# Optimization experiments

Measured on AMD Instinct MI355X. Metric: run time of the kernel, lower is better.

Reference implementation:

```python
import jax, jax.numpy as jnp
import numpy as np

B, C, T = 2, 64, 800
D, H, DH, FFD, L, NC = 128, 8, 64, 512, 2, 4
PL, NW = 25, 32            # patch_length, num_windows
WD = 0.1                   # window_duration
AHD = H * DH               # 512
SCALE = DH ** -0.5


def setup_inputs() -> dict:
    key = jax.random.key(0)
    ks = iter(jax.random.split(key, 40))
    def nrm(shape, s=0.02):
        return jax.random.normal(next(ks), shape, jnp.float32) * s
    return {
        "x_eeg": jax.random.normal(next(ks), (B, C, T), jnp.float32),
        "epoch_start_times": jax.random.uniform(next(ks), (B,), jnp.float32) * 10.0,
        "channel_voxel_indices": jax.random.randint(next(ks), (B, C), 0, 2048),
        "conv_w": nrm((D, PL), 0.1), "conv_b": nrm((D,), 0.01),
        "cls_token": nrm((1, 1, D), 1.0), "cls_pos": nrm((1, 1, D), 1.0),
        "bias_time_e": nrm((H, DH)), "bias_time_r": nrm((H, DH)),
        "bias_channel_r": nrm((H, DH)), "bias_channel_e": nrm((H, DH)),
        "ln1_g": jnp.ones((L, D)), "ln1_b": jnp.zeros((L, D)),
        "wqkv": nrm((L, D, 3 * AHD)), "wkt": nrm((L, D, AHD)), "wkc": nrm((L, D, AHD)),
        "wo": nrm((L, AHD, D)), "bo": jnp.zeros((L, D)),
        "ln2_g": jnp.ones((L, D)), "ln2_b": jnp.zeros((L, D)),
        "w1": nrm((L, D, FFD)), "b1": jnp.zeros((L, FFD)),
        "w2": nrm((L, FFD, D)), "b2": jnp.zeros((L, D)),
        "head_ln_g": jnp.ones((D,)), "head_ln_b": jnp.zeros((D,)),
        "head_w": nrm((D, NC)), "head_b": jnp.zeros((NC,)),
    }


def _ln(x, g, b, eps=1e-5):
    m = x.mean(-1, keepdims=True)
    v = ((x - m) ** 2).mean(-1, keepdims=True)
    return (x - m) / jnp.sqrt(v + eps) * g + b


def _posemb(p):
    # sinusoidal: outer product with inverse frequencies, concat(sin, cos)
    inv = 1.0 / (10000.0 ** (jnp.arange(0, D, 2, dtype=jnp.float32) / D))
    op = p[..., None] * inv
    return jnp.concatenate([jnp.sin(op), jnp.cos(op)], -1)


def reference(x_eeg, epoch_start_times, channel_voxel_indices, conv_w, conv_b,
              cls_token, cls_pos, bias_time_e, bias_time_r, bias_channel_r,
              bias_channel_e, ln1_g, ln1_b, wqkv, wkt, wkc, wo, bo,
              ln2_g, ln2_b, w1, b1, w2, b2, head_ln_g, head_ln_b, head_w, head_b):
    b = x_eeg.shape[0]
    # patch embedding: Conv2d(1->D, kernel (1,PL), stride (1,PL)) == per-window matmul
    xp = x_eeg.reshape(b, C, NW, PL)
    x = jnp.einsum('bcwp,dp->bcwd', xp, conv_w) + conv_b   # (b,C,NW,D)
    x = x.reshape(b, C * NW, D)                            # token order: c-major, matches flatten(2).T
    # positional embeddings
    tstart = jnp.floor(epoch_start_times / WD)             # '//' on float tensors = floor div
    tp = tstart[:, None] + jnp.arange(NW, dtype=jnp.float32)
    tpe = _posemb(tp)                                      # (b,NW,D)
    cpe = _posemb(channel_voxel_indices.astype(jnp.float32))  # (b,C,D)
    tpe = jnp.broadcast_to(tpe[:, None], (b, C, NW, D)).reshape(b, -1, D)
    cpe = jnp.broadcast_to(cpe[:, :, None], (b, C, NW, D)).reshape(b, -1, D)
    cls = jnp.broadcast_to(cls_token, (b, 1, D))
    clsp = jnp.broadcast_to(cls_pos, (b, 1, D))
    x = jnp.concatenate([cls, x], 1)
    r_t = jnp.concatenate([clsp, tpe], 1)
    r_c = jnp.concatenate([clsp, cpe], 1)
    n = x.shape[1]

    def tohead(t):
        # rearrange 'b n (h d) -> b h n d' then contiguous().view(n,b,h,d): flat reinterpretation
        return t.reshape(b, n, H, DH).transpose(0, 2, 1, 3).reshape(n, b, H, DH)

    for l in range(L):
        xn = _ln(x, ln1_g[l], ln1_b[l])
        q, k, v = jnp.split(xn @ wqkv[l], 3, -1)
        q, k, v = tohead(q), tohead(k), tohead(v)
        q_e = q + bias_time_e + bias_channel_e
        q_r = q + bias_time_r + bias_channel_r
        # k_r nets: (b,n,AHD).view(n,b,h,d) is a direct flat reshape in the source
        kt = (r_t @ wkt[l]).reshape(n, b, H, DH)
        kc = (r_c @ wkc[l]).reshape(n, b, H, DH)
        At = jnp.einsum('ibhd,jbhd->ijbh', q_e, k)
        Bt = jnp.einsum('ibhd,jbhd->ijbh', q_r, kt)
        Ct = jnp.einsum('ibhd,jbhd->ijbh', q_r, kc)
        # source uses nn.Softmax(dim=-1) on (i,j,b,h): normalizes over HEADS (faithful)
        att = jax.nn.softmax((At + Bt + Ct) * SCALE, axis=-1)
        o = jnp.einsum('ijbh,jbhd->ibhd', att, v)
        o = o.transpose(1, 0, 2, 3).reshape(b, n, AHD)     # 'n b h d -> b n (h d)'
        x = o @ wo[l] + bo[l] + x
        xn2 = _ln(x, ln2_g[l], ln2_b[l])
        hdn = jax.nn.gelu(xn2 @ w1[l] + b1[l], approximate=False)
        x = hdn @ w2[l] + b2[l] + x

    clsout = x[:, 0]                                       # pool='cls'
    return _ln(clsout, head_ln_g, head_ln_b) @ head_w + head_b
```

## Files before the change

kernel.cpp:

```cpp
#include <hip/hip_runtime.h>

#define CH    64
#define NTOK  2049
#define NTOKP 2064
#define MROWS 4098
#define NCJ   3

typedef __attribute__((ext_vector_type(8))) short bf16x8;
typedef __attribute__((ext_vector_type(4))) float f32x4;
typedef __attribute__((ext_vector_type(2))) int i32x2;

#define OFF_X     0u
#define OFF_XNB   524544u
#define OFF_RTB   786816u
#define OFF_RCB   1049088u
#define OFF_QKVB  1311360u
#define OFF_KTCB  4458624u
#define OFF_QNB   5507712u
#define OFF_KSB   6556800u
#define OFF_VNB   7613568u
#define OFF_VTB   8662656u
#define OFF_COLB  9727616u
#define OFF_WT    9760640u
#define OFF_OP    10284928u
#define OFF_ATTNO 13432192u
#define OFF_FFNH  14481280u

#define QSCALE 0.1803368801111204f

#define GLOAD_LDS16(gp, lp) __builtin_amdgcn_global_load_lds( \
    (const __attribute__((address_space(1))) void*)(gp), \
    (__attribute__((address_space(3))) void*)(lp), 16, 0, 0)

__device__ __forceinline__ float wave_allreduce_sum(float v) {
    #pragma unroll
    for (int m = 1; m < 64; m <<= 1) v += __shfl_xor(v, m);
    return v;
}

__device__ __forceinline__ ushort bf16rnd(float x) {
    unsigned u = __builtin_bit_cast(unsigned, x);
    u += 0x7FFF + ((u >> 16) & 1);
    return (ushort)(u >> 16);
}

__device__ __forceinline__ float bf16tof(ushort u) {
    return __builtin_bit_cast(float, ((unsigned)u) << 16);
}

__global__ __launch_bounds__(256) void wprep_kernel(
    const float* __restrict__ wqkv, const float* __restrict__ wkt, const float* __restrict__ wkc,
    const float* __restrict__ wo, const float* __restrict__ w1, const float* __restrict__ w2,
    ushort* __restrict__ wT)
{
    int l = blockIdx.z, mat = blockIdx.y;
    int idx = blockIdx.x * 256 + threadIdx.x;
    float v; int off;
    if (mat == 0) {
        if (idx >= 196608) return;
        int n = idx >> 7, k = idx & 127;
        v = wqkv[(size_t)l * 196608 + (size_t)k * 1536 + n]; off = 0;
    } else if (mat == 1) {
        if (idx >= 131072) return;
        int n = idx >> 8, k = idx & 255;
        v = (k < 128) ? wkt[(size_t)l * 65536 + (size_t)k * 512 + n]
                      : wkc[(size_t)l * 65536 + (size_t)(k - 128) * 512 + n];
        off = 196608;
    } else if (mat == 2) {
        if (idx >= 65536) return;
        int n = idx >> 9, k = idx & 511;
        v = wo[(size_t)l * 65536 + (size_t)k * 128 + n]; off = 327680;
    } else if (mat == 3) {
        if (idx >= 65536) return;
        int n = idx >> 7, k = idx & 127;
        v = w1[(size_t)l * 65536 + (size_t)k * 512 + n]; off = 393216;
    } else {
        if (idx >= 65536) return;
        int n = idx >> 9, k = idx & 511;
        v = w2[(size_t)l * 65536 + (size_t)k * 128 + n]; off = 458752;
    }
    wT[(size_t)l * 524288 + off + idx] = bf16rnd(v);
}

__global__ __launch_bounds__(128) void embed_kernel(
    const float* __restrict__ eeg, const float* __restrict__ est, const int* __restrict__ cvi,
    const float* __restrict__ cw, const float* __restrict__ cb,
    const float* __restrict__ cls, const float* __restrict__ clsp,
    float* __restrict__ x, ushort* __restrict__ rt, ushort* __restrict__ rc)
{
    int id = blockIdx.x;
    int d = threadIdx.x;
    if (id >= 4096) {
        int b = id - 4096;
        size_t base = (size_t)b * NTOK * 128 + d;
        x[base]  = cls[d];
        rt[base] = bf16rnd(clsp[d]);
        rc[base] = bf16rnd(clsp[d]);
        return;
    }
    int b = id >> 11, rem = id & 2047, c = rem >> 5, w = rem & 31;
    __shared__ float xs[25];
    if (d < 25) xs[d] = eeg[((size_t)(b * CH + c)) * 800 + w * 25 + d];
    __syncthreads();
    float acc = cb[d];
    #pragma unroll
    for (int p = 0; p < 25; ++p) acc += xs[p] * cw[d * 25 + p];
    int i = 1 + c * 32 + w;
    size_t base = ((size_t)b * NTOK + i) * 128 + d;
    x[base] = acc;
    int k = d & 63;
    float invk = __expf(-0.14391156831f * (float)k);
    float pt = floorf(est[b] / 0.1f) + (float)w;
    float at = pt * invk;
    rt[base] = bf16rnd((d < 64) ? sinf(at) : cosf(at));
    float pc = (float)cvi[b * CH + c];
    float ac = pc * invk;
    rc[base] = bf16rnd((d < 64) ? sinf(ac) : cosf(ac));
}

__global__ __launch_bounds__(256) void ln_kernel(
    const float* __restrict__ x, const float* __restrict__ g, const float* __restrict__ bb,
    ushort* __restrict__ out, int rows)
{
    int w = threadIdx.x >> 6, lane = threadIdx.x & 63;
    int row = blockIdx.x * 4 + w;
    if (row >= rows) return;
    const float* xr = x + (size_t)row * 128;
    float v0 = xr[lane], v1 = xr[lane + 64];
    float mean = wave_allreduce_sum(v0 + v1) * (1.0f / 128.0f);
    float d0 = v0 - mean, d1 = v1 - mean;
    float var = wave_allreduce_sum(d0 * d0 + d1 * d1) * (1.0f / 128.0f);
    float inv = rsqrtf(var + 1e-5f);
    out[(size_t)row * 128 + lane]      = bf16rnd(d0 * inv * g[lane]      + bb[lane]);
    out[(size_t)row * 128 + lane + 64] = bf16rnd(d1 * inv * g[lane + 64] + bb[lane + 64]);
}

__global__ __launch_bounds__(256, 3) void mgemm_kernel(
    const ushort* __restrict__ A, const ushort* __restrict__ A2, int K1,
    const ushort* __restrict__ Wt,
    float* outF, ushort* outB, const float* bias, const float* res,
    int M, int K, int N, int mode)
{
    __shared__ ushort Alds[128 * 72];
    __shared__ ushort Blds[128 * 72];
    int tid = threadIdx.x;
    int lane = tid & 63, wv = tid >> 6;
    int wm = wv >> 1, wn = wv & 1;
    int li = lane & 15, g = lane >> 4;
    int m0 = blockIdx.y * 128, n0 = blockIdx.x * 128;
    int K2s = K - K1;
    f32x4 acc[4][4];
    #pragma unroll
    for (int a = 0; a < 4; ++a)
        #pragma unroll
        for (int c = 0; c < 4; ++c) acc[a][c] = (f32x4){0.f, 0.f, 0.f, 0.f};

    for (int kb = 0; kb < K; kb += 64) {
        #pragma unroll
        for (int it = 0; it < 4; ++it) {
            int gi = tid + it * 256;
            int row = gi >> 3, gc = gi & 7;
            int m = m0 + row; if (m >= M) m = M - 1;
            int acol = kb + gc * 8;
            const ushort* asrc = (acol < K1) ? (A + (size_t)m * K1 + acol)
                                             : (A2 + (size_t)m * K2s + (acol - K1));
            bf16x8 av = *(const bf16x8*)asrc;
            *(bf16x8*)&Alds[row * 72 + ((gc ^ (row & 7)) << 3)] = av;
            int n = n0 + row;
            bf16x8 bv = *(const bf16x8*)(Wt + (size_t)n * K + acol);
            *(bf16x8*)&Blds[row * 72 + ((gc ^ (row & 7)) << 3)] = bv;
        }
        __syncthreads();
        #pragma unroll
        for (int k2 = 0; k2 < 2; ++k2) {
            bf16x8 af[4], bfr[4];
            #pragma unroll
            for (int xx = 0; xx < 4; ++xx) {
                int ra = wm * 64 + xx * 16 + li;
                int rb = wn * 64 + xx * 16 + li;
                af[xx]  = *(const bf16x8*)&Alds[ra * 72 + (((k2 * 4 + g) ^ (ra & 7)) << 3)];
                bfr[xx] = *(const bf16x8*)&Blds[rb * 72 + (((k2 * 4 + g) ^ (rb & 7)) << 3)];
            }
            #pragma unroll
            for (int mi = 0; mi < 4; ++mi)
                #pragma unroll
                for (int ni = 0; ni < 4; ++ni)
                    acc[mi][ni] = __builtin_amdgcn_mfma_f32_16x16x32_bf16(af[mi], bfr[ni], acc[mi][ni], 0, 0, 0);
        }
        __syncthreads();
    }
    #pragma unroll
    for (int mi = 0; mi < 4; ++mi) {
        #pragma unroll
        for (int r = 0; r < 4; ++r) {
            int m = m0 + wm * 64 + mi * 16 + 4 * g + r;
            if (m >= M) continue;
            #pragma unroll
            for (int ni = 0; ni < 4; ++ni) {
                int n = n0 + wn * 64 + ni * 16 + li;
                float v = acc[mi][ni][r];
                if (mode == 2) {
                    v += bias[n];
                    v = 0.5f * v * (1.0f + erff(v * 0.70710678118f));
                    outB[(size_t)m * N + n] = bf16rnd(v);
                } else {
                    outB[(size_t)m * N + n] = bf16rnd(v);
                }
            }
        }
    }
}

__global__ __launch_bounds__(256) void tgemm_kernel(
    const ushort* __restrict__ A, const ushort* __restrict__ Wt,
    float* __restrict__ outF, const float* __restrict__ bias, const float* __restrict__ res,
    int M, int N)
{
    int lane = threadIdx.x & 63, wv = threadIdx.x >> 6;
    int li = lane & 15, g = lane >> 4;
    int mt = blockIdx.y * 4 + wv;
    int m0 = mt * 16, n0 = blockIdx.x * 16;
    int ar = m0 + li; if (ar >= M) ar = M - 1;
    const ushort* arow = A + (size_t)ar * 512 + 8 * g;
    const ushort* brow = Wt + (size_t)(n0 + li) * 512 + 8 * g;
    f32x4 acc = (f32x4){0.f, 0.f, 0.f, 0.f};
    #pragma unroll
    for (int k2 = 0; k2 < 16; ++k2) {
        bf16x8 af = *(const bf16x8*)(arow + k2 * 32);
        bf16x8 bf = *(const bf16x8*)(brow + k2 * 32);
        acc = __builtin_amdgcn_mfma_f32_16x16x32_bf16(af, bf, acc, 0, 0, 0);
    }
    #pragma unroll
    for (int r = 0; r < 4; ++r) {
        int m = m0 + 4 * g + r;
        if (m < M) {
            int n = n0 + li;
            outF[(size_t)m * N + n] = acc[r] + bias[n] + res[(size_t)m * N + n];
        }
    }
}

__global__ __launch_bounds__(512) void remap_kernel(
    const ushort* __restrict__ qkvb, const ushort* __restrict__ ktcb,
    const float* __restrict__ bte, const float* __restrict__ btr,
    const float* __restrict__ bcr, const float* __restrict__ bce,
    ushort* __restrict__ qn, ushort* __restrict__ ksum, ushort* __restrict__ vn,
    float* __restrict__ colb)
{
    int id = blockIdx.x;
    int b2 = id / NTOK, i2 = id - b2 * NTOK;
    int t = threadIdx.x;
    int h2 = t >> 6, d2 = t & 63;
    int G = i2 * 16 + b2 * 8 + h2;
    int bhA = G / 2049, iA = G - bhA * 2049;
    int bA = bhA >> 3, hA = bhA & 7;
    size_t qbase = ((size_t)(bA * NTOK + iA)) * 1536 + hA * 64 + d2;
    ushort qv = qkvb[qbase], kvu = qkvb[qbase + 512], vvu = qkvb[qbase + 1024];
    int bB = G / 16392, remB = G - bB * 16392;
    int iB = remB >> 3, hB = remB & 7;
    ushort ktcu = ktcb[((size_t)(bB * NTOK + iB)) * 512 + hB * 64 + d2];
    float kv = bf16tof(kvu), ktcv = bf16tof(ktcu);
    qn[(size_t)id * 512 + t] = bf16rnd(bf16tof(qv) * QSCALE);
    ksum[((size_t)(b2 * NTOKP + i2)) * 512 + t] = bf16rnd(kv + ktcv);
    vn[(size_t)id * 512 + t] = vvu;
    float cbx = (bte[t] + bce[t]) * kv + (btr[t] + bcr[t]) * ktcv;
    cbx = wave_allreduce_sum(cbx);
    if (d2 == 0) colb[((size_t)(b2 * NTOKP + i2)) * 8 + h2] = cbx;
}

__global__ __launch_bounds__(256) void vtrans_kernel(
    const ushort* __restrict__ vn, ushort* __restrict__ vt)
{
    __shared__ ushort tile[32][36];
    int jt = blockIdx.x, dt = blockIdx.y, b = blockIdx.z;
    int t = threadIdx.x;
    {
        int jj = t >> 3, dq = t & 7;
        int j = jt * 32 + jj;
        ushort4 v = make_ushort4(0, 0, 0, 0);
        if (j <= 2048)
            v = *(const ushort4*)(vn + ((size_t)(b * NTOK + j)) * 512 + dt * 32 + dq * 4);
        *(ushort4*)&tile[jj][dq * 4] = v;
    }
    __syncthreads();
    {
        int dd = t >> 3, jq = t & 7;
        ushort4 w;
        w.x = tile[jq * 4 + 0][dd];
        w.y = tile[jq * 4 + 1][dd];
        w.z = tile[jq * 4 + 2][dd];
        w.w = tile[jq * 4 + 3][dd];
        *(ushort4*)(vt + ((size_t)b * 512 + dt * 32 + dd) * 2080 + jt * 32 + jq * 4) = w;
    }
}

__global__ __launch_bounds__(256, 2) void attn9_kernel(
    const ushort* __restrict__ qn, const ushort* __restrict__ ks,
    const ushort* __restrict__ vt, const float* __restrict__ colb,
    ushort* __restrict__ Op)
{
    __shared__ __align__(16) char smem[71168];
    const int tid = threadIdx.x;
    const int lane = tid & 63, wv = tid >> 6;
    const int wi = wv >> 1, hg = wv & 1;
    const int g = lane >> 4, li = lane & 15;
    const int nc = blockIdx.y, b = blockIdx.z;
    const int i0 = blockIdx.x * 32;
    const int jt0 = nc * 43, jt1 = (nc + 1) * 43;

    bf16x8 qf[4][2];
    {
        int iq = i0 + wi * 16 + li; if (iq > 2048) iq = 2048;
        const ushort* qrow = qn + ((size_t)(b * NTOK + iq)) * 512 + hg * 256;
        #pragma unroll
        for (int hh = 0; hh < 4; ++hh)
            #pragma unroll
            for (int k2 = 0; k2 < 2; ++k2)
                qf[hh][k2] = *(const bf16x8*)(qrow + hh * 64 + k2 * 32 + 8 * g);
    }
    f32x4 o[4][4];
    #pragma unroll
    for (int a = 0; a < 4; ++a)
        #pragma unroll
        for (int m = 0; m < 4; ++m) o[a][m] = (f32x4){0.f, 0.f, 0.f, 0.f};

    const unsigned koff0 = (unsigned)(li * 1024) + (unsigned)((g * 16) ^ ((li & 7) << 4))
                         + (unsigned)(hg * 512);
    const unsigned koff1 = (unsigned)(li * 1024) + (unsigned)((64 + g * 16) ^ ((li & 7) << 4))
                         + (unsigned)(hg * 512);
    const unsigned vboff = (unsigned)(li * 32)
                         + (unsigned)((((g >> 1) ^ ((li >> 2) & 1)) << 4) + (g & 1) * 8)
                         + (unsigned)(hg * 8192);
    const unsigned exoff = 67072u + (unsigned)(wv * 1024 + lane * 16);
    const unsigned exoffp = 67072u + (unsigned)((wv ^ 1) * 1024 + lane * 16);

    const ushort* ksb_b = ks + ((size_t)b * NTOKP) * 512;
    auto stageK = [&](int jt, int buf) {
        #pragma unroll
        for (int t = 0; t < 4; ++t) {
            unsigned L = (unsigned)((wv * 256 + t * 64 + lane) * 16);
            unsigned Lp = L ^ (((L >> 10) & 7u) << 4);
            const ushort* src = ksb_b + (size_t)(jt * 16 + (int)(Lp >> 10)) * 512 + ((Lp & 1023u) >> 1);
            GLOAD_LDS16(src, smem + buf * 16384 + (wv * 256 + t * 64) * 16);
        }
    };
    const ushort* vtb_b = vt + (size_t)b * 512 * 2080;
    auto stageV = [&](int jt, int buf) {
        #pragma unroll
        for (int t = 0; t < 4; ++t) {
            int n = wv * 256 + t * 64 + lane;
            int d = n >> 1;
            int h16 = (n & 1) ^ ((n >> 3) & 1);
            const ushort* src = vtb_b + (size_t)d * 2080 + jt * 16 + h16 * 8;
            GLOAD_LDS16(src, smem + 32768 + buf * 16384 + (wv * 256 + t * 64) * 16);
        }
    };
    auto loadcb = [&](int jt) -> float {
        if (tid < 128) {
            int jg = jt * 16 + (tid >> 3);
            if (jg > 2063) jg = 2063;
            return colb[((size_t)(b * NTOKP + jg)) * 8 + (tid & 7)] * QSCALE;
        }
        return 0.f;
    };

    stageK(jt0, 0); stageV(jt0, 0);
    {
        float c0 = loadcb(jt0);
        if (tid < 128) ((float*)(smem + 65536))[(tid >> 3) * 12 + (tid & 7)] = c0;
    }
    float cbreg = loadcb(jt0 + 1);

    int cur = 0;
    for (int jt = jt0; jt < jt1; ++jt) {
        __syncthreads();
        const char* kb = smem + cur * 16384;
        f32x4 s[4];
        #pragma unroll
        for (int hh = 0; hh < 4; ++hh) {
            s[hh] = (f32x4){0.f, 0.f, 0.f, 0.f};
            bf16x8 kf0 = *(const bf16x8*)(kb + koff0 + hh * 128);
            s[hh] = __builtin_amdgcn_mfma_f32_16x16x32_bf16(kf0, qf[hh][0], s[hh], 0, 0, 0);
            bf16x8 kf1 = *(const bf16x8*)(kb + koff1 + hh * 128);
            s[hh] = __builtin_amdgcn_mfma_f32_16x16x32_bf16(kf1, qf[hh][1], s[hh], 0, 0, 0);
        }
        const float* cbl = (const float*)(smem + 65536 + cur * 768);
        float p[4][4];
        #pragma unroll
        for (int rp = 0; rp < 2; ++rp) {
            f32x4 ce = *(const f32x4*)(cbl + (4 * g + 2 * rp) * 12 + hg * 4);
            f32x4 co = *(const f32x4*)(cbl + (4 * g + 2 * rp) * 12 + 12 + hg * 4);
            #pragma unroll
            for (int hh = 0; hh < 4; ++hh) {
                p[hh][2 * rp]     = __builtin_amdgcn_exp2f(s[hh][2 * rp]     + ce[hh]);
                p[hh][2 * rp + 1] = __builtin_amdgcn_exp2f(s[hh][2 * rp + 1] + co[hh]);
            }
        }
        f32x4 e;
        #pragma unroll
        for (int r = 0; r < 4; ++r)
            e[r] = (p[0][r] + p[1][r]) + (p[2][r] + p[3][r]);
        *(f32x4*)(smem + exoff) = e;
        __syncthreads();
        f32x4 eo = *(const f32x4*)(smem + exoffp);
        const bool hn = (jt + 1 < jt1);
        if (hn) {
            if (tid < 128) ((float*)(smem + 65536 + (cur ^ 1) * 768))[(tid >> 3) * 12 + (tid & 7)] = cbreg;
            stageK(jt + 1, cur ^ 1);
            stageV(jt + 1, cur ^ 1);
            cbreg = loadcb(jt + 2);
        }
        float inv[4];
        #pragma unroll
        for (int r = 0; r < 4; ++r)
            inv[r] = __builtin_amdgcn_rcpf(fmaxf(e[r] + eo[r], 1e-20f));
        unsigned P2[4][2];
        #pragma unroll
        for (int hh = 0; hh < 4; ++hh)
            #pragma unroll
            for (int rp = 0; rp < 2; ++rp) {
                float lo = p[hh][2 * rp] * inv[2 * rp];
                float hi = p[hh][2 * rp + 1] * inv[2 * rp + 1];
                asm("v_cvt_pk_bf16_f32 %0, %1, %2" : "=v"(P2[hh][rp]) : "v"(lo), "v"(hi));
            }
        const char* vb = smem + 32768 + cur * 16384 + vboff;
        #pragma unroll
        for (int hh = 0; hh < 4; ++hh) {
            i32x2 pa = (i32x2){(int)P2[hh][0], (int)P2[hh][1]};
            #pragma unroll
            for (int dt = 0; dt < 4; ++dt) {
                i32x2 vv = *(const i32x2*)(vb + hh * 2048 + dt * 512);
                asm("v_mfma_f32_16x16x16_bf16 %0, %1, %2, %0"
                    : "+a"(o[hh][dt]) : "v"(pa), "v"(vv));
            }
        }
        cur ^= 1;
    }
    {
        int irow0 = i0 + wi * 16 + 4 * g;
        #pragma unroll
        for (int hh = 0; hh < 4; ++hh) {
            int d0 = (hg * 4 + hh) * 64;
            #pragma unroll
            for (int dt = 0; dt < 4; ++dt) {
                #pragma unroll
                for (int r = 0; r < 4; ++r) {
                    int irow = irow0 + r;
                    if (irow <= 2048) {
                        Op[(((size_t)(nc * 2 + b)) * 2049 + irow) * 512 + d0 + dt * 16 + li] =
                            bf16rnd(o[hh][dt][r]);
                    }
                }
            }
        }
    }
}

__global__ __launch_bounds__(256) void osum_kernel(
    const ushort* __restrict__ Op, ushort* __restrict__ attno)
{
    int idx = blockIdx.x * 256 + threadIdx.x;
    if (idx >= MROWS * 64) return;
    int row = idx >> 6, dq = idx & 63;
    int b = row / NTOK, i = row - b * NTOK;
    float acc[8];
    #pragma unroll
    for (int e = 0; e < 8; ++e) acc[e] = 0.f;
    #pragma unroll
    for (int nc = 0; nc < NCJ; ++nc) {
        const ushort* src = Op + (((size_t)(nc * 2 + b)) * 2049 + i) * 512 + dq * 8;
        int4 v = *(const int4*)src;
        const ushort* up = (const ushort*)&v;
        #pragma unroll
        for (int e = 0; e < 8; ++e) acc[e] += bf16tof(up[e]);
    }
    ushort ov[8];
    #pragma unroll
    for (int e = 0; e < 8; ++e) ov[e] = bf16rnd(acc[e]);
    *(int4*)(attno + (size_t)row * 512 + dq * 8) = *(int4*)ov;
}

__global__ void head_kernel(
    const float* __restrict__ x, const float* __restrict__ g, const float* __restrict__ b,
    const float* __restrict__ w, const float* __restrict__ hb, float* __restrict__ out)
{
    int lane = threadIdx.x & 63;
    for (int bi = 0; bi < 2; ++bi) {
        const float* xr = x + (size_t)bi * NTOK * 128;
        float v0 = xr[lane], v1 = xr[lane + 64];
        float mean = wave_allreduce_sum(v0 + v1) * (1.0f / 128.0f);
        float d0 = v0 - mean, d1 = v1 - mean;
        float var = wave_allreduce_sum(d0 * d0 + d1 * d1) * (1.0f / 128.0f);
        float inv = rsqrtf(var + 1e-5f);
        float y0 = d0 * inv * g[lane] + b[lane];
        float y1 = d1 * inv * g[lane + 64] + b[lane + 64];
        for (int c = 0; c < 4; ++c) {
            float pt = y0 * w[lane * 4 + c] + y1 * w[(lane + 64) * 4 + c];
            pt = wave_allreduce_sum(pt);
            if (lane == 0) out[bi * 4 + c] = pt + hb[c];
        }
    }
}

extern "C" void kernel_launch(void* const* d_in, const int* in_sizes, int n_in,
                              void* d_out, int out_size, void* d_ws, size_t ws_size,
                              hipStream_t stream) {
    const float* eeg   = (const float*)d_in[0];
    const float* est   = (const float*)d_in[1];
    const int*   cvi   = (const int*)d_in[2];
    const float* convw = (const float*)d_in[3];
    const float* convb = (const float*)d_in[4];
    const float* cls   = (const float*)d_in[5];
    const float* clsp  = (const float*)d_in[6];
    const float* bte   = (const float*)d_in[7];
    const float* btr   = (const float*)d_in[8];
    const float* bcr   = (const float*)d_in[9];
    const float* bce   = (const float*)d_in[10];
    const float* ln1g  = (const float*)d_in[11];
    const float* ln1b  = (const float*)d_in[12];
    const float* wqkv  = (const float*)d_in[13];
    const float* wkt   = (const float*)d_in[14];
    const float* wkc   = (const float*)d_in[15];
    const float* wo    = (const float*)d_in[16];
    const float* bo    = (const float*)d_in[17];
    const float* ln2g  = (const float*)d_in[18];
    const float* ln2b  = (const float*)d_in[19];
    const float* w1    = (const float*)d_in[20];
    const float* b1    = (const float*)d_in[21];
    const float* w2    = (const float*)d_in[22];
    const float* b2    = (const float*)d_in[23];
    const float* hlng  = (const float*)d_in[24];
    const float* hlnb  = (const float*)d_in[25];
    const float* hw    = (const float*)d_in[26];
    const float* hb    = (const float*)d_in[27];

    float* ws    = (float*)d_ws;
    float* x_    = ws + OFF_X;
    ushort* xnb  = (ushort*)(ws + OFF_XNB);
    ushort* rtb  = (ushort*)(ws + OFF_RTB);
    ushort* rcb  = (ushort*)(ws + OFF_RCB);
    ushort* qkvb = (ushort*)(ws + OFF_QKVB);
    ushort* ktcb = (ushort*)(ws + OFF_KTCB);
    ushort* qnb  = (ushort*)(ws + OFF_QNB);
    ushort* ksb  = (ushort*)(ws + OFF_KSB);
    ushort* vnb  = (ushort*)(ws + OFF_VNB);
    ushort* vtb  = (ushort*)(ws + OFF_VTB);
    float* colb_ = ws + OFF_COLB;
    ushort* wT   = (ushort*)(ws + OFF_WT);
    ushort* opb  = (ushort*)(ws + OFF_OP);
    ushort* attnob = (ushort*)(ws + OFF_ATTNO);
    ushort* ffnhb  = (ushort*)(ws + OFF_FFNH);

    for (int b = 0; b < 2; ++b) {
        hipMemsetAsync(ksb + ((size_t)(b * NTOKP + 2049)) * 512, 0,
                       (NTOKP - 2049) * 512 * sizeof(ushort), stream);
        hipMemsetAsync(colb_ + ((size_t)(b * NTOKP + 2049)) * 8, 0,
                       (NTOKP - 2049) * 8 * sizeof(float), stream);
    }

    wprep_kernel<<<dim3(768, 5, 2), 256, 0, stream>>>(wqkv, wkt, wkc, wo, w1, w2, wT);
    embed_kernel<<<4098, 128, 0, stream>>>(eeg, est, cvi, convw, convb, cls, clsp, x_, rtb, rcb);

    for (int l = 0; l < 2; ++l) {
        const ushort* wTl = wT + (size_t)l * 524288;
        ln_kernel<<<1025, 256, 0, stream>>>(x_, ln1g + l * 128, ln1b + l * 128, xnb, MROWS);
        mgemm_kernel<<<dim3(12, 33), 256, 0, stream>>>(xnb, xnb, 128, wTl,
                                                       nullptr, qkvb, nullptr, nullptr,
                                                       MROWS, 128, 1536, 3);
        mgemm_kernel<<<dim3(4, 33), 256, 0, stream>>>(rtb, rcb, 128, wTl + 196608,
                                                      nullptr, ktcb, nullptr, nullptr,
                                                      MROWS, 256, 512, 3);
        remap_kernel<<<MROWS, 512, 0, stream>>>(qkvb, ktcb, bte, btr, bcr, bce,
                                                qnb, ksb, vnb, colb_);
        vtrans_kernel<<<dim3(65, 16, 2), 256, 0, stream>>>(vnb, vtb);
        attn9_kernel<<<dim3(65, NCJ, 2), 256, 0, stream>>>(qnb, ksb, vtb, colb_, opb);
        osum_kernel<<<1025, 256, 0, stream>>>(opb, attnob);
        tgemm_kernel<<<dim3(8, 65), 256, 0, stream>>>(attnob, wTl + 327680, x_,
                                                      bo + l * 128, x_, MROWS, 128);
        ln_kernel<<<1025, 256, 0, stream>>>(x_, ln2g + l * 128, ln2b + l * 128, xnb, MROWS);
        mgemm_kernel<<<dim3(4, 33), 256, 0, stream>>>(xnb, xnb, 128, wTl + 393216,
                                                      nullptr, ffnhb, b1 + l * 512, nullptr,
                                                      MROWS, 128, 512, 2);
        tgemm_kernel<<<dim3(8, 65), 256, 0, stream>>>(ffnhb, wTl + 458752, x_,
                                                      b2 + l * 128, x_, MROWS, 128);
    }
    head_kernel<<<1, 64, 0, stream>>>(x_, hlng, hlnb, hw, hb, (float*)d_out);
}
```

Measured before the change: 355.1 us.

## Fuse partial-sum reduction into output GEMM, load K from registers, hoist k-proj GEMMs

Removes the osum kernel by having a new tgemm3 kernel sum the three split-J partial attention outputs while loading its A operand. The attention kernel now reads K fragments directly from global memory into registers, prefetched one tile ahead, instead of staging K through LDS. This cuts LDS use so more blocks may fit per CU, but it adds global-load latency to the inner loop. Both per-layer relative-key projection GEMMs are hoisted ahead of the layer loop into separate buffers, since they depend only on the embedding outputs.

```diff
diff --git a/kernel.cpp b/kernel.cpp
--- a/kernel.cpp
+++ b/kernel.cpp
@@ -23,7 +23,7 @@
 #define OFF_COLB  9727616u
 #define OFF_WT    9760640u
 #define OFF_OP    10284928u
-#define OFF_ATTNO 13432192u
+#define OFF_KTCB2 13432192u
 #define OFF_FFNH  14481280u
 
 #define QSCALE 0.1803368801111204f
@@ -240,6 +240,47 @@
     }
 }
 
+__global__ __launch_bounds__(256) void tgemm3_kernel(
+    const ushort* __restrict__ Op, const ushort* __restrict__ Wt,
+    float* __restrict__ outF, const float* __restrict__ bias, const float* __restrict__ res,
+    int M, int N)
+{
+    int lane = threadIdx.x & 63, wv = threadIdx.x >> 6;
+    int li = lane & 15, g = lane >> 4;
+    int mt = blockIdx.y * 4 + wv;
+    int m0 = mt * 16, n0 = blockIdx.x * 16;
+    int ar = m0 + li; if (ar >= M) ar = M - 1;
+    int bb = (ar >= NTOK) ? 1 : 0;
+    int ii = ar - bb * NTOK;
+    const ushort* a0 = Op + (((size_t)(0 * 2 + bb)) * 2049 + ii) * 512 + 8 * g;
+    const ushort* a1 = Op + (((size_t)(1 * 2 + bb)) * 2049 + ii) * 512 + 8 * g;
+    const ushort* a2 = Op + (((size_t)(2 * 2 + bb)) * 2049 + ii) * 512 + 8 * g;
+    const ushort* brow = Wt + (size_t)(n0 + li) * 512 + 8 * g;
+    f32x4 acc = (f32x4){0.f, 0.f, 0.f, 0.f};
+    #pragma unroll
+    for (int k2 = 0; k2 < 16; ++k2) {
+        bf16x8 x0 = *(const bf16x8*)(a0 + k2 * 32);
+        bf16x8 x1 = *(const bf16x8*)(a1 + k2 * 32);
+        bf16x8 x2 = *(const bf16x8*)(a2 + k2 * 32);
+        bf16x8 af;
+        #pragma unroll
+        for (int e = 0; e < 8; ++e) {
+            float sv = bf16tof((ushort)x0[e]) + bf16tof((ushort)x1[e]) + bf16tof((ushort)x2[e]);
+            af[e] = (short)bf16rnd(sv);
+        }
+        bf16x8 bf = *(const bf16x8*)(brow + k2 * 32);
+        acc = __builtin_amdgcn_mfma_f32_16x16x32_bf16(af, bf, acc, 0, 0, 0);
+    }
+    #pragma unroll
+    for (int r = 0; r < 4; ++r) {
+        int m = m0 + 4 * g + r;
+        if (m < M) {
+            int n = n0 + li;
+            outF[(size_t)m * N + n] = acc[r] + bias[n] + res[(size_t)m * N + n];
+        }
+    }
+}
+
 __global__ __launch_bounds__(512) void remap_kernel(
     const ushort* __restrict__ qkvb, const ushort* __restrict__ ktcb,
     const float* __restrict__ bte, const float* __restrict__ btr,
@@ -294,12 +335,12 @@
     }
 }
 
-__global__ __launch_bounds__(256, 2) void attn9_kernel(
+__global__ __launch_bounds__(256, 2) void attn10_kernel(
     const ushort* __restrict__ qn, const ushort* __restrict__ ks,
     const ushort* __restrict__ vt, const float* __restrict__ colb,
     ushort* __restrict__ Op)
 {
-    __shared__ __align__(16) char smem[71168];
+    __shared__ __align__(16) char smem[38400];
     const int tid = threadIdx.x;
     const int lane = tid & 63, wv = tid >> 6;
     const int wi = wv >> 1, hg = wv & 1;
@@ -324,26 +365,14 @@
         #pragma unroll
         for (int m = 0; m < 4; ++m) o[a][m] = (f32x4){0.f, 0.f, 0.f, 0.f};
 
-    const unsigned koff0 = (unsigned)(li * 1024) + (unsigned)((g * 16) ^ ((li & 7) << 4))
-                         + (unsigned)(hg * 512);
-    const unsigned koff1 = (unsigned)(li * 1024) + (unsigned)((64 + g * 16) ^ ((li & 7) << 4))
-                         + (unsigned)(hg * 512);
+    const ushort* kbase = ks + ((size_t)b * NTOKP + li) * 512 + hg * 256 + 8 * g;
+
     const unsigned vboff = (unsigned)(li * 32)
                          + (unsigned)((((g >> 1) ^ ((li >> 2) & 1)) << 4) + (g & 1) * 8)
                          + (unsigned)(hg * 8192);
-    const unsigned exoff = 67072u + (unsigned)(wv * 1024 + lane * 16);
-    const unsigned exoffp = 67072u + (unsigned)((wv ^ 1) * 1024 + lane * 16);
-
-    const ushort* ksb_b = ks + ((size_t)b * NTOKP) * 512;
-    auto stageK = [&](int jt, int buf) {
-        #pragma unroll
-        for (int t = 0; t < 4; ++t) {
-            unsigned L = (unsigned)((wv * 256 + t * 64 + lane) * 16);
-            unsigned Lp = L ^ (((L >> 10) & 7u) << 4);
-            const ushort* src = ksb_b + (size_t)(jt * 16 + (int)(Lp >> 10)) * 512 + ((Lp & 1023u) >> 1);
-            GLOAD_LDS16(src, smem + buf * 16384 + (wv * 256 + t * 64) * 16);
-        }
-    };
+    const unsigned exoff  = 34304u + (unsigned)(wv * 1024 + lane * 16);
+    const unsigned exoffp = 34304u + (unsigned)((wv ^ 1) * 1024 + lane * 16);
+
     const ushort* vtb_b = vt + (size_t)b * 512 * 2080;
     auto stageV = [&](int jt, int buf) {
         #pragma unroll
@@ -352,7 +381,7 @@
             int d = n >> 1;
             int h16 = (n & 1) ^ ((n >> 3) & 1);
             const ushort* src = vtb_b + (size_t)d * 2080 + jt * 16 + h16 * 8;
-            GLOAD_LDS16(src, smem + 32768 + buf * 16384 + (wv * 256 + t * 64) * 16);
+            GLOAD_LDS16(src, smem + buf * 16384 + (wv * 256 + t * 64) * 16);
         }
     };
     auto loadcb = [&](int jt) -> float {
@@ -364,27 +393,32 @@
         return 0.f;
     };
 
-    stageK(jt0, 0); stageV(jt0, 0);
+    bf16x8 kc[8];
+    {
+        const ushort* kp = kbase + (size_t)(jt0 * 16) * 512;
+        #pragma unroll
+        for (int q = 0; q < 8; ++q)
+            kc[q] = *(const bf16x8*)(kp + (q >> 1) * 64 + (q & 1) * 32);
+    }
+    stageV(jt0, 0);
     {
         float c0 = loadcb(jt0);
-        if (tid < 128) ((float*)(smem + 65536))[(tid >> 3) * 12 + (tid & 7)] = c0;
+        if (tid < 128) ((float*)(smem + 32768))[(tid >> 3) * 12 + (tid & 7)] = c0;
     }
     float cbreg = loadcb(jt0 + 1);
 
     int cur = 0;
+    #pragma unroll 2
     for (int jt = jt0; jt < jt1; ++jt) {
         __syncthreads();
-        const char* kb = smem + cur * 16384;
         f32x4 s[4];
         #pragma unroll
         for (int hh = 0; hh < 4; ++hh) {
             s[hh] = (f32x4){0.f, 0.f, 0.f, 0.f};
-            bf16x8 kf0 = *(const bf16x8*)(kb + koff0 + hh * 128);
-            s[hh] = __builtin_amdgcn_mfma_f32_16x16x32_bf16(kf0, qf[hh][0], s[hh], 0, 0, 0);
-            bf16x8 kf1 = *(const bf16x8*)(kb + koff1 + hh * 128);
-            s[hh] = __builtin_amdgcn_mfma_f32_16x16x32_bf16(kf1, qf[hh][1], s[hh], 0, 0, 0);
-        }
-        const float* cbl = (const float*)(smem + 65536 + cur * 768);
+            s[hh] = __builtin_amdgcn_mfma_f32_16x16x32_bf16(kc[hh * 2 + 0], qf[hh][0], s[hh], 0, 0, 0);
+            s[hh] = __builtin_amdgcn_mfma_f32_16x16x32_bf16(kc[hh * 2 + 1], qf[hh][1], s[hh], 0, 0, 0);
+        }
+        const float* cbl = (const float*)(smem + 32768 + cur * 768);
         float p[4][4];
         #pragma unroll
         for (int rp = 0; rp < 2; ++rp) {
@@ -405,10 +439,17 @@
         f32x4 eo = *(const f32x4*)(smem + exoffp);
         const bool hn = (jt + 1 < jt1);
         if (hn) {
-            if (tid < 128) ((float*)(smem + 65536 + (cur ^ 1) * 768))[(tid >> 3) * 12 + (tid & 7)] = cbreg;
-            stageK(jt + 1, cur ^ 1);
+            if (tid < 128) ((float*)(smem + 32768 + (cur ^ 1) * 768))[(tid >> 3) * 12 + (tid & 7)] = cbreg;
             stageV(jt + 1, cur ^ 1);
             cbreg = loadcb(jt + 2);
+        }
+        bf16x8 kn[8];
+        {
+            int jn = jt + 1; if (jn > 128) jn = 128;
+            const ushort* kp = kbase + (size_t)(jn * 16) * 512;
+            #pragma unroll
+            for (int q = 0; q < 8; ++q)
+                kn[q] = *(const bf16x8*)(kp + (q >> 1) * 64 + (q & 1) * 32);
         }
         float inv[4];
         #pragma unroll
@@ -423,7 +464,7 @@
                 float hi = p[hh][2 * rp + 1] * inv[2 * rp + 1];
                 asm("v_cvt_pk_bf16_f32 %0, %1, %2" : "=v"(P2[hh][rp]) : "v"(lo), "v"(hi));
             }
-        const char* vb = smem + 32768 + cur * 16384 + vboff;
+        const char* vb = smem + cur * 16384 + vboff;
         #pragma unroll
         for (int hh = 0; hh < 4; ++hh) {
             i32x2 pa = (i32x2){(int)P2[hh][0], (int)P2[hh][1]};
@@ -434,6 +475,8 @@
                     : "+a"(o[hh][dt]) : "v"(pa), "v"(vv));
             }
         }
+        #pragma unroll
+        for (int q = 0; q < 8; ++q) kc[q] = kn[q];
         cur ^= 1;
     }
     {
@@ -454,30 +497,6 @@
             }
         }
     }
-}
-
-__global__ __launch_bounds__(256) void osum_kernel(
-    const ushort* __restrict__ Op, ushort* __restrict__ attno)
-{
-    int idx = blockIdx.x * 256 + threadIdx.x;
-    if (idx >= MROWS * 64) return;
-    int row = idx >> 6, dq = idx & 63;
-    int b = row / NTOK, i = row - b * NTOK;
-    float acc[8];
-    #pragma unroll
-    for (int e = 0; e < 8; ++e) acc[e] = 0.f;
-    #pragma unroll
-    for (int nc = 0; nc < NCJ; ++nc) {
-        const ushort* src = Op + (((size_t)(nc * 2 + b)) * 2049 + i) * 512 + dq * 8;
-        int4 v = *(const int4*)src;
-        const ushort* up = (const ushort*)&v;
-        #pragma unroll
-        for (int e = 0; e < 8; ++e) acc[e] += bf16tof(up[e]);
-    }
-    ushort ov[8];
-    #pragma unroll
-    for (int e = 0; e < 8; ++e) ov[e] = bf16rnd(acc[e]);
-    *(int4*)(attno + (size_t)row * 512 + dq * 8) = *(int4*)ov;
 }
 
 __global__ void head_kernel(
@@ -540,7 +559,8 @@
     ushort* rtb  = (ushort*)(ws + OFF_RTB);
     ushort* rcb  = (ushort*)(ws + OFF_RCB);
     ushort* qkvb = (ushort*)(ws + OFF_QKVB);
-    ushort* ktcb = (ushort*)(ws + OFF_KTCB);
+    ushort* ktcb0 = (ushort*)(ws + OFF_KTCB);
+    ushort* ktcb1 = (ushort*)(ws + OFF_KTCB2);
     ushort* qnb  = (ushort*)(ws + OFF_QNB);
     ushort* ksb  = (ushort*)(ws + OFF_KSB);
     ushort* vnb  = (ushort*)(ws + OFF_VNB);
@@ -548,7 +568,6 @@
     float* colb_ = ws + OFF_COLB;
     ushort* wT   = (ushort*)(ws + OFF_WT);
     ushort* opb  = (ushort*)(ws + OFF_OP);
-    ushort* attnob = (ushort*)(ws + OFF_ATTNO);
     ushort* ffnhb  = (ushort*)(ws + OFF_FFNH);
 
     for (int b = 0; b < 2; ++b) {
@@ -561,22 +580,26 @@
     wprep_kernel<<<dim3(768, 5, 2), 256, 0, stream>>>(wqkv, wkt, wkc, wo, w1, w2, wT);
     embed_kernel<<<4098, 128, 0, stream>>>(eeg, est, cvi, convw, convb, cls, clsp, x_, rtb, rcb);
 
+    mgemm_kernel<<<dim3(4, 33), 256, 0, stream>>>(rtb, rcb, 128, wT + 196608,
+                                                  nullptr, ktcb0, nullptr, nullptr,
+                                                  MROWS, 256, 512, 3);
+    mgemm_kernel<<<dim3(4, 33), 256, 0, stream>>>(rtb, rcb, 128, wT + 524288 + 196608,
+                                                  nullptr, ktcb1, nullptr, nullptr,
+                                                  MROWS, 256, 512, 3);
+
     for (int l = 0; l < 2; ++l) {
         const ushort* wTl = wT + (size_t)l * 524288;
+        ushort* ktcb_l = (l == 0) ? ktcb0 : ktcb1;
         ln_kernel<<<1025, 256, 0, stream>>>(x_, ln1g + l * 128, ln1b + l * 128, xnb, MROWS);
         mgemm_kernel<<<dim3(12, 33), 256, 0, stream>>>(xnb, xnb, 128, wTl,
                                                        nullptr, qkvb, nullptr, nullptr,
                                                        MROWS, 128, 1536, 3);
-        mgemm_kernel<<<dim3(4, 33), 256, 0, stream>>>(rtb, rcb, 128, wTl + 196608,
-                                                      nullptr, ktcb, nullptr, nullptr,
-                                                      MROWS, 256, 512, 3);
-        remap_kernel<<<MROWS, 512, 0, stream>>>(qkvb, ktcb, bte, btr, bcr, bce,
+        remap_kernel<<<MROWS, 512, 0, stream>>>(qkvb, ktcb_l, bte, btr, bcr, bce,
                                                 qnb, ksb, vnb, colb_);
         vtrans_kernel<<<dim3(65, 16, 2), 256, 0, stream>>>(vnb, vtb);
-        attn9_kernel<<<dim3(65, NCJ, 2), 256, 0, stream>>>(qnb, ksb, vtb, colb_, opb);
-        osum_kernel<<<1025, 256, 0, stream>>>(opb, attnob);
-        tgemm_kernel<<<dim3(8, 65), 256, 0, stream>>>(attnob, wTl + 327680, x_,
-                                                      bo + l * 128, x_, MROWS, 128);
+        attn10_kernel<<<dim3(65, NCJ, 2), 256, 0, stream>>>(qnb, ksb, vtb, colb_, opb);
+        tgemm3_kernel<<<dim3(8, 65), 256, 0, stream>>>(opb, wTl + 327680, x_,
+                                                       bo + l * 128, x_, MROWS, 128);
         ln_kernel<<<1025, 256, 0, stream>>>(x_, ln2g + l * 128, ln2b + l * 128, xnb, MROWS);
         mgemm_kernel<<<dim3(4, 33), 256, 0, stream>>>(xnb, xnb, 128, wTl + 393216,
                                                       nullptr, ffnhb, b1 + l * 512, nullptr,
```

After: 440.6 us. +24.1%, slower.

## Single-buffer attention LDS, split keys four ways, hoist relative-key GEMMs

Applied to the files above, without the earlier changes.

The attention kernel drops K/V double-buffering and uses one LDS buffer for each, cutting shared memory from about 71KB to 37KB so more blocks can be resident per CU. V is now staged at the top of each iteration and K for the next tile during softmax, which reduces overlap of loads with compute. The key-chunk split goes from 3 to 4 to give more blocks. The relative-position key GEMMs for both layers are moved out of the layer loop since they depend only on embeddings, and workspace buffers are aliased. Aliasing opb chunk count with NCJ=4 may overflow the OFF_OP region, since the per-chunk partial output buffer grows.

```diff
diff --git a/kernel.cpp b/kernel.cpp
--- a/kernel.cpp
+++ b/kernel.cpp
@@ -4,7 +4,7 @@
 #define NTOK  2049
 #define NTOKP 2064
 #define MROWS 4098
-#define NCJ   3
+#define NCJ   4
 
 typedef __attribute__((ext_vector_type(8))) short bf16x8;
 typedef __attribute__((ext_vector_type(4))) float f32x4;
@@ -23,8 +23,7 @@
 #define OFF_COLB  9727616u
 #define OFF_WT    9760640u
 #define OFF_OP    10284928u
-#define OFF_ATTNO 13432192u
-#define OFF_FFNH  14481280u
+#define OFF_KTCB2 14481280u
 
 #define QSCALE 0.1803368801111204f
 
@@ -294,19 +293,19 @@
     }
 }
 
-__global__ __launch_bounds__(256, 2) void attn9_kernel(
+__global__ __launch_bounds__(256, 2) void attn11_kernel(
     const ushort* __restrict__ qn, const ushort* __restrict__ ks,
     const ushort* __restrict__ vt, const float* __restrict__ colb,
     ushort* __restrict__ Op)
 {
-    __shared__ __align__(16) char smem[71168];
+    __shared__ __align__(16) char smem[37632];
     const int tid = threadIdx.x;
     const int lane = tid & 63, wv = tid >> 6;
     const int wi = wv >> 1, hg = wv & 1;
     const int g = lane >> 4, li = lane & 15;
     const int nc = blockIdx.y, b = blockIdx.z;
     const int i0 = blockIdx.x * 32;
-    const int jt0 = nc * 43, jt1 = (nc + 1) * 43;
+    const int jt0 = (nc * 129) / NCJ, jt1 = ((nc + 1) * 129) / NCJ;
 
     bf16x8 qf[4][2];
     {
@@ -328,31 +327,31 @@
                          + (unsigned)(hg * 512);
     const unsigned koff1 = (unsigned)(li * 1024) + (unsigned)((64 + g * 16) ^ ((li & 7) << 4))
                          + (unsigned)(hg * 512);
-    const unsigned vboff = (unsigned)(li * 32)
+    const unsigned vboff = 16384u + (unsigned)(li * 32)
                          + (unsigned)((((g >> 1) ^ ((li >> 2) & 1)) << 4) + (g & 1) * 8)
                          + (unsigned)(hg * 8192);
-    const unsigned exoff = 67072u + (unsigned)(wv * 1024 + lane * 16);
-    const unsigned exoffp = 67072u + (unsigned)((wv ^ 1) * 1024 + lane * 16);
+    const unsigned exoff  = 33536u + (unsigned)(wv * 1024 + lane * 16);
+    const unsigned exoffp = 33536u + (unsigned)((wv ^ 1) * 1024 + lane * 16);
 
     const ushort* ksb_b = ks + ((size_t)b * NTOKP) * 512;
-    auto stageK = [&](int jt, int buf) {
+    auto stageK = [&](int jt) {
         #pragma unroll
         for (int t = 0; t < 4; ++t) {
             unsigned L = (unsigned)((wv * 256 + t * 64 + lane) * 16);
             unsigned Lp = L ^ (((L >> 10) & 7u) << 4);
             const ushort* src = ksb_b + (size_t)(jt * 16 + (int)(Lp >> 10)) * 512 + ((Lp & 1023u) >> 1);
-            GLOAD_LDS16(src, smem + buf * 16384 + (wv * 256 + t * 64) * 16);
+            GLOAD_LDS16(src, smem + (wv * 256 + t * 64) * 16);
         }
     };
     const ushort* vtb_b = vt + (size_t)b * 512 * 2080;
-    auto stageV = [&](int jt, int buf) {
+    auto stageV = [&](int jt) {
         #pragma unroll
         for (int t = 0; t < 4; ++t) {
             int n = wv * 256 + t * 64 + lane;
             int d = n >> 1;
             int h16 = (n & 1) ^ ((n >> 3) & 1);
             const ushort* src = vtb_b + (size_t)d * 2080 + jt * 16 + h16 * 8;
-            GLOAD_LDS16(src, smem + 32768 + buf * 16384 + (wv * 256 + t * 64) * 16);
+            GLOAD_LDS16(src, smem + 16384 + (wv * 256 + t * 64) * 16);
         }
     };
     auto loadcb = [&](int jt) -> float {
@@ -364,27 +363,26 @@
         return 0.f;
     };
 
-    stageK(jt0, 0); stageV(jt0, 0);
+    stageK(jt0);
     {
         float c0 = loadcb(jt0);
-        if (tid < 128) ((float*)(smem + 65536))[(tid >> 3) * 12 + (tid & 7)] = c0;
+        if (tid < 128) ((float*)(smem + 32768))[(tid >> 3) * 12 + (tid & 7)] = c0;
     }
     float cbreg = loadcb(jt0 + 1);
 
-    int cur = 0;
     for (int jt = jt0; jt < jt1; ++jt) {
         __syncthreads();
-        const char* kb = smem + cur * 16384;
+        stageV(jt);
         f32x4 s[4];
         #pragma unroll
         for (int hh = 0; hh < 4; ++hh) {
             s[hh] = (f32x4){0.f, 0.f, 0.f, 0.f};
-            bf16x8 kf0 = *(const bf16x8*)(kb + koff0 + hh * 128);
+            bf16x8 kf0 = *(const bf16x8*)(smem + koff0 + hh * 128);
             s[hh] = __builtin_amdgcn_mfma_f32_16x16x32_bf16(kf0, qf[hh][0], s[hh], 0, 0, 0);
-            bf16x8 kf1 = *(const bf16x8*)(kb + koff1 + hh * 128);
+            bf16x8 kf1 = *(const bf16x8*)(smem + koff1 + hh * 128);
             s[hh] = __builtin_amdgcn_mfma_f32_16x16x32_bf16(kf1, qf[hh][1], s[hh], 0, 0, 0);
         }
-        const float* cbl = (const float*)(smem + 65536 + cur * 768);
+        const float* cbl = (const float*)(smem + 32768);
         float p[4][4];
         #pragma unroll
         for (int rp = 0; rp < 2; ++rp) {
@@ -405,9 +403,8 @@
         f32x4 eo = *(const f32x4*)(smem + exoffp);
         const bool hn = (jt + 1 < jt1);
         if (hn) {
-            if (tid < 128) ((float*)(smem + 65536 + (cur ^ 1) * 768))[(tid >> 3) * 12 + (tid & 7)] = cbreg;
-            stageK(jt + 1, cur ^ 1);
-            stageV(jt + 1, cur ^ 1);
+            if (tid < 128) ((float*)(smem + 32768))[(tid >> 3) * 12 + (tid & 7)] = cbreg;
+            stageK(jt + 1);
             cbreg = loadcb(jt + 2);
         }
         float inv[4];
@@ -423,18 +420,16 @@
                 float hi = p[hh][2 * rp + 1] * inv[2 * rp + 1];
                 asm("v_cvt_pk_bf16_f32 %0, %1, %2" : "=v"(P2[hh][rp]) : "v"(lo), "v"(hi));
             }
-        const char* vb = smem + 32768 + cur * 16384 + vboff;
         #pragma unroll
         for (int hh = 0; hh < 4; ++hh) {
             i32x2 pa = (i32x2){(int)P2[hh][0], (int)P2[hh][1]};
             #pragma unroll
             for (int dt = 0; dt < 4; ++dt) {
-                i32x2 vv = *(const i32x2*)(vb + hh * 2048 + dt * 512);
+                i32x2 vv = *(const i32x2*)(smem + vboff + hh * 2048 + dt * 512);
                 asm("v_mfma_f32_16x16x16_bf16 %0, %1, %2, %0"
                     : "+a"(o[hh][dt]) : "v"(pa), "v"(vv));
             }
         }
-        cur ^= 1;
     }
     {
         int irow0 = i0 + wi * 16 + 4 * g;
@@ -540,7 +535,8 @@
     ushort* rtb  = (ushort*)(ws + OFF_RTB);
     ushort* rcb  = (ushort*)(ws + OFF_RCB);
     ushort* qkvb = (ushort*)(ws + OFF_QKVB);
-    ushort* ktcb = (ushort*)(ws + OFF_KTCB);
+    ushort* ktcb0 = (ushort*)(ws + OFF_KTCB);
+    ushort* ktcb1 = (ushort*)(ws + OFF_KTCB2);
     ushort* qnb  = (ushort*)(ws + OFF_QNB);
     ushort* ksb  = (ushort*)(ws + OFF_KSB);
     ushort* vnb  = (ushort*)(ws + OFF_VNB);
@@ -548,8 +544,8 @@
     float* colb_ = ws + OFF_COLB;
     ushort* wT   = (ushort*)(ws + OFF_WT);
     ushort* opb  = (ushort*)(ws + OFF_OP);
-    ushort* attnob = (ushort*)(ws + OFF_ATTNO);
-    ushort* ffnhb  = (ushort*)(ws + OFF_FFNH);
+    ushort* attnob = vnb;
+    ushort* ffnhb  = qnb;
 
     for (int b = 0; b < 2; ++b) {
         hipMemsetAsync(ksb + ((size_t)(b * NTOKP + 2049)) * 512, 0,
@@ -561,19 +557,24 @@
     wprep_kernel<<<dim3(768, 5, 2), 256, 0, stream>>>(wqkv, wkt, wkc, wo, w1, w2, wT);
     embed_kernel<<<4098, 128, 0, stream>>>(eeg, est, cvi, convw, convb, cls, clsp, x_, rtb, rcb);
 
+    mgemm_kernel<<<dim3(4, 33), 256, 0, stream>>>(rtb, rcb, 128, wT + 196608,
+                                                  nullptr, ktcb0, nullptr, nullptr,
+                                                  MROWS, 256, 512, 3);
+    mgemm_kernel<<<dim3(4, 33), 256, 0, stream>>>(rtb, rcb, 128, wT + 524288 + 196608,
+                                                  nullptr, ktcb1, nullptr, nullptr,
+                                                  MROWS, 256, 512, 3);
+
     for (int l = 0; l < 2; ++l) {
         const ushort* wTl = wT + (size_t)l * 524288;
+        ushort* ktcb_l = (l == 0) ? ktcb0 : ktcb1;
         ln_kernel<<<1025, 256, 0, stream>>>(x_, ln1g + l * 128, ln1b + l * 128, xnb, MROWS);
         mgemm_kernel<<<dim3(12, 33), 256, 0, stream>>>(xnb, xnb, 128, wTl,
                                                        nullptr, qkvb, nullptr, nullptr,
                                                        MROWS, 128, 1536, 3);
-        mgemm_kernel<<<dim3(4, 33), 256, 0, stream>>>(rtb, rcb, 128, wTl + 196608,
-                                                      nullptr, ktcb, nullptr, nullptr,
-                                                      MROWS, 256, 512, 3);
-        remap_kernel<<<MROWS, 512, 0, stream>>>(qkvb, ktcb, bte, btr, bcr, bce,
+        remap_kernel<<<MROWS, 512, 0, stream>>>(qkvb, ktcb_l, bte, btr, bcr, bce,
                                                 qnb, ksb, vnb, colb_);
         vtrans_kernel<<<dim3(65, 16, 2), 256, 0, stream>>>(vnb, vtb);
-        attn9_kernel<<<dim3(65, NCJ, 2), 256, 0, stream>>>(qnb, ksb, vtb, colb_, opb);
+        attn11_kernel<<<dim3(65, NCJ, 2), 256, 0, stream>>>(qnb, ksb, vtb, colb_, opb);
         osum_kernel<<<1025, 256, 0, stream>>>(opb, attnob);
         tgemm_kernel<<<dim3(8, 65), 256, 0, stream>>>(attnob, wTl + 327680, x_,
                                                       bo + l * 128, x_, MROWS, 128);
```

Result: slower. 413.5 us (+16.5%).
